# Kernel tuning notes

Hardware: AMD Instinct MI355X
Metric: run time of the kernel (lower is better)

The kernel has to match this reference:

```python
import math
import jax, jax.numpy as jnp
import numpy as np

D = 2048
NH = 16
HD = D // NH
B_IMG = 32
H_ORIG, W_ORIG = 28, 36
POOL = 2
HF, WF = H_ORIG // POOL, W_ORIG // POOL  # 14, 18
T = HF * WF                              # 252 tokens per image
S_TOTAL = B_IMG * T                      # 8064
EPS = 1e-6


def setup_inputs() -> dict:
    key = jax.random.key(0)
    ks = jax.random.split(key, 12)
    w = lambda k, shp: jax.random.normal(k, shp, dtype=jnp.float32) * 0.02
    return {
        'semantic_hidden': jax.random.normal(ks[0], (1, S_TOTAL, D), jnp.float32),
        'vggt_features': jax.random.normal(ks[1], (1, S_TOTAL, D), jnp.float32),
        'grid_thw': jnp.tile(jnp.array([[1, H_ORIG, W_ORIG]], dtype=jnp.int64), (B_IMG, 1)),
        'ln1_w': jnp.ones((D,), jnp.float32), 'ln1_b': jnp.zeros((D,), jnp.float32),
        'ln2_w': jnp.ones((D,), jnp.float32), 'ln2_b': jnp.zeros((D,), jnp.float32),
        'Wq': w(ks[2], (D, D)), 'Wk': w(ks[3], (D, D)),
        'Wv': w(ks[4], (D, D)), 'Wo': w(ks[5], (D, D)),
        'imp_w1': w(ks[6], (D // 4, D)), 'imp_b1': jnp.zeros((D // 4,), jnp.float32),
        'imp_w2': w(ks[7], (1, D // 4)), 'imp_b2': jnp.zeros((1,), jnp.float32),
        'gate_w': w(ks[8], (NH // 2, D)), 'gate_b': jnp.zeros((NH // 2,), jnp.float32),
        'gate': jnp.asarray(0.5, jnp.float32),  # torch init is 0.0 (output would be all-zero); use 0.5 for a meaningful baseline
    }


def _layernorm(x, w, b):
    mu = jnp.mean(x, axis=-1, keepdims=True)
    var = jnp.var(x, axis=-1, keepdims=True)
    return (x - mu) * jax.lax.rsqrt(var + EPS) * w + b


def _spatial_bias(h_feat, w_feat, dtype):
    y = jnp.arange(h_feat, dtype=dtype)
    x = jnp.arange(w_feat, dtype=dtype)
    gy, gx = jnp.meshgrid(y, x, indexing='ij')
    coords = jnp.stack([gy.reshape(-1), gx.reshape(-1)], axis=-1)  # [N, 2]
    diff = coords[:, None, :] - coords[None, :, :]
    dist = jnp.sqrt(jnp.sum(diff * diff, axis=-1))  # [N, N]
    diag_len = math.sqrt(h_feat ** 2 + w_feat ** 2) + 1e-6
    return -dist / diag_len


def reference(semantic_hidden, vggt_features, grid_thw, ln1_w, ln1_b, ln2_w, ln2_b,
              Wq, Wk, Wv, Wo, imp_w1, imp_b1, imp_w2, imp_b2, gate_w, gate_b, gate):
    sem = _layernorm(semantic_hidden, ln1_w, ln1_b)
    vgg = _layernorm(vggt_features, ln2_w, ln2_b)
    B_orig, S_total, Dm = sem.shape

    # grid_thw is a static host constant -> Python ints (shapes must be static)
    h_feat = int(np.asarray(grid_thw)[0, 1]) // POOL
    w_feat = int(np.asarray(grid_thw)[0, 2]) // POOL
    tokens = h_feat * w_feat
    num_images = S_total // tokens

    q_in = sem.reshape(num_images, tokens, Dm)   # [B, S, D]
    kv_in = vgg.reshape(num_images, tokens, Dm)
    B, S = num_images, tokens

    q = (q_in @ Wq.T).reshape(B, S, NH, HD).transpose(0, 2, 1, 3)   # [B, H, S, hd]
    k = (kv_in @ Wk.T).reshape(B, S, NH, HD).transpose(0, 2, 1, 3)
    v = (kv_in @ Wv.T).reshape(B, S, NH, HD).transpose(0, 2, 1, 3)

    attn = jnp.einsum('bhqd,bhkd->bhqk', q, k) / math.sqrt(HD)       # [B, H, S, S]

    # spatial bias on first half of heads, gated per (image, query)
    sp_bias = _spatial_bias(h_feat, w_feat, q.dtype)                 # [S, S]
    gate_score = jax.nn.sigmoid(q_in @ gate_w.T + gate_b)            # [B, S, H/2]
    gate_score = gate_score.transpose(0, 2, 1)[..., None]            # [B, H/2, S, 1]
    split = NH // 2
    attn = attn.at[:, :split].add(sp_bias[None, None] * gate_score)

    # importance gate: log-importance bias over keys, shared across heads
    hidden = jax.nn.relu(q_in @ imp_w1.T + imp_b1)
    importance = jax.nn.sigmoid(hidden @ imp_w2.T + imp_b2)          # [B, S, 1]
    attn = attn + jnp.log(importance + 0.1).reshape(B, 1, 1, S)

    probs = jax.nn.softmax(attn, axis=-1)
    out = jnp.einsum('bhqk,bhkd->bhqd', probs, v)                    # [B, H, S, hd]
    out = out.transpose(0, 2, 1, 3).reshape(B, S, Dm)
    out = out.reshape(B_orig, S_total, Dm) @ Wo.T
    return jnp.tanh(gate) * out
```

## Files before the change

### kernel.cpp

```cpp
#include <hip/hip_runtime.h>
#include <hip/hip_bf16.h>
#include <math.h>

typedef __bf16 bf16_t;
typedef __bf16 bf16x8 __attribute__((ext_vector_type(8)));
typedef float f32x4v __attribute__((ext_vector_type(4)));
typedef unsigned short ushort_t;

#define SL_TOTAL 8064
#define SL_PAD 8192
#define DMODEL 2048
#define NHEAD 16
#define HDIM 128
#define SEQ 252

__device__ __forceinline__ bf16_t f2bf(float f) {
  unsigned u = __builtin_bit_cast(unsigned, f);
  u += 0x7fffu + ((u >> 16) & 1u);
  ushort_t h = (ushort_t)(u >> 16);
  return __builtin_bit_cast(bf16_t, h);
}
__device__ __forceinline__ float bf2f(bf16_t b) {
  unsigned u = ((unsigned)__builtin_bit_cast(ushort_t, b)) << 16;
  return __builtin_bit_cast(float, u);
}

__global__ __launch_bounds__(256) void cvt4_kernel(const float* __restrict__ s0,
                                                   const float* __restrict__ s1,
                                                   const float* __restrict__ s2,
                                                   const float* __restrict__ s3,
                                                   bf16_t* __restrict__ d0,
                                                   bf16_t* __restrict__ d1,
                                                   bf16_t* __restrict__ d2,
                                                   bf16_t* __restrict__ d3) {
  const float* src; bf16_t* dst;
  switch (blockIdx.y) {
    case 0: src = s0; dst = d0; break;
    case 1: src = s1; dst = d1; break;
    case 2: src = s2; dst = d2; break;
    default: src = s3; dst = d3; break;
  }
  int i = (blockIdx.x * 256 + threadIdx.x) * 8;
  float4 a = *(const float4*)(src + i);
  float4 b = *(const float4*)(src + i + 4);
  bf16x8 o;
  o[0] = f2bf(a.x); o[1] = f2bf(a.y); o[2] = f2bf(a.z); o[3] = f2bf(a.w);
  o[4] = f2bf(b.x); o[5] = f2bf(b.y); o[6] = f2bf(b.z); o[7] = f2bf(b.w);
  *(bf16x8*)(dst + i) = o;
}

__global__ __launch_bounds__(256) void cvt_kernel(const float* __restrict__ src,
                                                  bf16_t* __restrict__ dst, int n) {
  int i = (blockIdx.x * 256 + threadIdx.x) * 8;
  if (i >= n) return;
  float4 a = *(const float4*)(src + i);
  float4 b = *(const float4*)(src + i + 4);
  bf16x8 o;
  o[0] = f2bf(a.x); o[1] = f2bf(a.y); o[2] = f2bf(a.z); o[3] = f2bf(a.w);
  o[4] = f2bf(b.x); o[5] = f2bf(b.y); o[6] = f2bf(b.z); o[7] = f2bf(b.w);
  *(bf16x8*)(dst + i) = o;
}

__global__ __launch_bounds__(256) void ln_kernel(
    const float* __restrict__ sem, const float* __restrict__ vgg,
    const float* __restrict__ w1, const float* __restrict__ b1,
    const float* __restrict__ w2, const float* __restrict__ b2,
    bf16_t* __restrict__ o1, bf16_t* __restrict__ o2) {
  const float* x; const float* w; const float* bb; bf16_t* o;
  int row = blockIdx.x;
  if (blockIdx.y == 0) { x = sem; w = w1; bb = b1; o = o1; }
  else                 { x = vgg; w = w2; bb = b2; o = o2; }
  x += (size_t)row * DMODEL; o += (size_t)row * DMODEL;
  int t = threadIdx.x, wid = t >> 6, lane = t & 63;
  float4 va = *(const float4*)(x + t * 8);
  float4 vb = *(const float4*)(x + t * 8 + 4);
  float s  = va.x + va.y + va.z + va.w + vb.x + vb.y + vb.z + vb.w;
  float ss = va.x*va.x + va.y*va.y + va.z*va.z + va.w*va.w
           + vb.x*vb.x + vb.y*vb.y + vb.z*vb.z + vb.w*vb.w;
  #pragma unroll
  for (int m = 1; m < 64; m <<= 1) { s += __shfl_xor(s, m); ss += __shfl_xor(ss, m); }
  __shared__ float rs[4], rss[4];
  if (lane == 0) { rs[wid] = s; rss[wid] = ss; }
  __syncthreads();
  float st = rs[0] + rs[1] + rs[2] + rs[3];
  float sst = rss[0] + rss[1] + rss[2] + rss[3];
  float mu = st * (1.0f / 2048.0f);
  float var = sst * (1.0f / 2048.0f) - mu * mu;
  float rstd = rsqrtf(var + 1e-6f);
  float4 wa = *(const float4*)(w + t * 8);
  float4 wb = *(const float4*)(w + t * 8 + 4);
  float4 ba = *(const float4*)(bb + t * 8);
  float4 bb4 = *(const float4*)(bb + t * 8 + 4);
  bf16x8 ov;
  ov[0] = f2bf((va.x - mu) * rstd * wa.x + ba.x);
  ov[1] = f2bf((va.y - mu) * rstd * wa.y + ba.y);
  ov[2] = f2bf((va.z - mu) * rstd * wa.z + ba.z);
  ov[3] = f2bf((va.w - mu) * rstd * wa.w + ba.w);
  ov[4] = f2bf((vb.x - mu) * rstd * wb.x + bb4.x);
  ov[5] = f2bf((vb.y - mu) * rstd * wb.y + bb4.y);
  ov[6] = f2bf((vb.z - mu) * rstd * wb.z + bb4.z);
  ov[7] = f2bf((vb.w - mu) * rstd * wb.w + bb4.w);
  *(bf16x8*)(o + t * 8) = ov;
}

template <int EPI>
__global__ __launch_bounds__(512, 2) void gemm256(
    const bf16_t* __restrict__ A, const bf16_t* __restrict__ B,
    void* __restrict__ C, void* __restrict__ C2,
    const float* __restrict__ gatep,
    int Mreal, int N, int K, int nnt) {
  __shared__ bf16_t As[2][256 * 64];
  __shared__ bf16_t Bs[2][256 * 64];
  const int nblk = gridDim.x;
  const int orig = blockIdx.x;
  const int qd = nblk >> 3, rr = nblk & 7, xc = orig & 7, lin = orig >> 3;
  const int wg = (xc < rr ? xc * (qd + 1) : rr * (qd + 1) + (xc - rr) * qd) + lin;
  const int mtile = wg / nnt, ntile = wg - mtile * nnt;
  const int m0 = mtile * 256, n0 = ntile * 256;

  const int tid = threadIdx.x;
  const int wid = tid >> 6, lane = tid & 63;
  const int l15 = lane & 15, l4 = lane >> 4;
  const int wr = wid >> 2, wc = wid & 3;
  const int srow = lane >> 3;
  const int scol = 8 * ((lane & 7) ^ srow);

  f32x4v acc[8][4] = {};
  const int NKT = K >> 6;

  auto stage_all = [&](int kt, bf16_t* an, bf16_t* bn) {
    const int k0 = kt << 6;
    #pragma unroll
    for (int it = 0; it < 4; ++it) {
      int chunk = wid + 8 * it;
      int row = chunk * 8 + srow;
      const bf16_t* ga = A + (size_t)(m0 + row) * K + k0 + scol;
      __builtin_amdgcn_global_load_lds((const __attribute__((address_space(1))) unsigned int*)ga,
          (__attribute__((address_space(3))) unsigned int*)(an + chunk * 512), 16, 0, 0);
    }
    #pragma unroll
    for (int it = 0; it < 4; ++it) {
      int chunk = wid + 8 * it;
      int row = chunk * 8 + srow;
      const bf16_t* gb = B + (size_t)(n0 + row) * K + k0 + scol;
      __builtin_amdgcn_global_load_lds((const __attribute__((address_space(1))) unsigned int*)gb,
          (__attribute__((address_space(3))) unsigned int*)(bn + chunk * 512), 16, 0, 0);
    }
  };

  auto ld_a = [&](const bf16_t* as, int ks, int mi) -> bf16x8 {
    int row = wr * 128 + mi * 16 + l15;
    int cb = ks * 64 + l4 * 16;
    return *(const bf16x8*)((const char*)as + row * 128 + (cb ^ ((row & 7) << 4)));
  };
  auto ld_b = [&](const bf16_t* bs, int ks, int ni) -> bf16x8 {
    int row = wc * 64 + ni * 16 + l15;
    int cb = ks * 64 + l4 * 16;
    return *(const bf16x8*)((const char*)bs + row * 128 + (cb ^ ((row & 7) << 4)));
  };

  auto tile_step = [&](int t, const bf16_t* as, const bf16_t* bs,
                       bf16_t* an, bf16_t* bn) {
    bf16x8 af[4], bfv[4];
    #pragma unroll
    for (int mi = 0; mi < 4; ++mi) af[mi] = ld_a(as, 0, mi);
    #pragma unroll
    for (int ni = 0; ni < 4; ++ni) bfv[ni] = ld_b(bs, 0, ni);
    if (t + 1 < NKT) stage_all(t + 1, an, bn);
    __builtin_amdgcn_s_barrier();
    asm volatile("s_waitcnt lgkmcnt(0)" ::: "memory");
    __builtin_amdgcn_sched_barrier(0);
    __builtin_amdgcn_s_setprio(1);
    #pragma unroll
    for (int mi = 0; mi < 4; ++mi)
      #pragma unroll
      for (int ni = 0; ni < 4; ++ni)
        acc[mi][ni] = __builtin_amdgcn_mfma_f32_16x16x32_bf16(af[mi], bfv[ni], acc[mi][ni], 0, 0, 0);
    __builtin_amdgcn_s_setprio(0);
    __builtin_amdgcn_s_barrier();
    __builtin_amdgcn_sched_barrier(0);
    #pragma unroll
    for (int mi = 0; mi < 4; ++mi) af[mi] = ld_a(as, 0, mi + 4);
    __builtin_amdgcn_s_barrier();
    asm volatile("s_waitcnt lgkmcnt(0)" ::: "memory");
    __builtin_amdgcn_sched_barrier(0);
    __builtin_amdgcn_s_setprio(1);
    #pragma unroll
    for (int mi = 0; mi < 4; ++mi)
      #pragma unroll
      for (int ni = 0; ni < 4; ++ni)
        acc[mi + 4][ni] = __builtin_amdgcn_mfma_f32_16x16x32_bf16(af[mi], bfv[ni], acc[mi + 4][ni], 0, 0, 0);
    __builtin_amdgcn_s_setprio(0);
    __builtin_amdgcn_s_barrier();
    __builtin_amdgcn_sched_barrier(0);
    #pragma unroll
    for (int mi = 0; mi < 4; ++mi) af[mi] = ld_a(as, 1, mi);
    #pragma unroll
    for (int ni = 0; ni < 4; ++ni) bfv[ni] = ld_b(bs, 1, ni);
    __builtin_amdgcn_s_barrier();
    asm volatile("s_waitcnt lgkmcnt(0)" ::: "memory");
    __builtin_amdgcn_sched_barrier(0);
    __builtin_amdgcn_s_setprio(1);
    #pragma unroll
    for (int mi = 0; mi < 4; ++mi)
      #pragma unroll
      for (int ni = 0; ni < 4; ++ni)
        acc[mi][ni] = __builtin_amdgcn_mfma_f32_16x16x32_bf16(af[mi], bfv[ni], acc[mi][ni], 0, 0, 0);
    __builtin_amdgcn_s_setprio(0);
    __builtin_amdgcn_s_barrier();
    __builtin_amdgcn_sched_barrier(0);
    #pragma unroll
    for (int mi = 0; mi < 4; ++mi) af[mi] = ld_a(as, 1, mi + 4);
    __builtin_amdgcn_s_barrier();
    asm volatile("s_waitcnt lgkmcnt(0)" ::: "memory");
    __builtin_amdgcn_sched_barrier(0);
    __builtin_amdgcn_s_setprio(1);
    #pragma unroll
    for (int mi = 0; mi < 4; ++mi)
      #pragma unroll
      for (int ni = 0; ni < 4; ++ni)
        acc[mi + 4][ni] = __builtin_amdgcn_mfma_f32_16x16x32_bf16(af[mi], bfv[ni], acc[mi + 4][ni], 0, 0, 0);
    __builtin_amdgcn_s_setprio(0);
    if (t + 1 < NKT) asm volatile("s_waitcnt vmcnt(0)" ::: "memory");
    __builtin_amdgcn_s_barrier();
    __builtin_amdgcn_sched_barrier(0);
  };

  stage_all(0, As[0], Bs[0]);
  asm volatile("s_waitcnt vmcnt(0)" ::: "memory");
  __builtin_amdgcn_s_barrier();
  __builtin_amdgcn_sched_barrier(0);

  for (int t = 0; t < NKT; t += 2) {
    tile_step(t,     As[0], Bs[0], As[1], Bs[1]);
    tile_step(t + 1, As[1], Bs[1], As[0], Bs[0]);
  }

  float scale = 1.0f;
  if (EPI == 2) scale = tanhf(gatep[0]);
  bf16_t* Cb = (bf16_t*)C;
  int colbase = n0;
  int ldc = N;
  if (EPI == 3) {
    ldc = 2048;
    if (n0 >= 2048) { Cb = (bf16_t*)C2; colbase = n0 - 2048; }
  }
  #pragma unroll
  for (int mi = 0; mi < 8; ++mi) {
    #pragma unroll
    for (int ni = 0; ni < 4; ++ni) {
      int c = colbase + wc * 64 + ni * 16 + l15;
      #pragma unroll
      for (int j = 0; j < 4; ++j) {
        int r = m0 + wr * 128 + mi * 16 + 4 * l4 + j;
        if (r >= Mreal) continue;
        float v = acc[mi][ni][j];
        if (EPI == 2) ((float*)C)[(size_t)r * N + c] = v * scale;
        else Cb[(size_t)r * ldc + c] = f2bf(v);
      }
    }
  }
}

template <int EPI>
__global__ __launch_bounds__(256, 2) void gemm_bt(
    const bf16_t* __restrict__ A, const bf16_t* __restrict__ B,
    void* __restrict__ C, void* __restrict__ C2,
    const float* __restrict__ bias, const float* __restrict__ gatep,
    int M, int N, int K, int nnt) {
  __shared__ bf16_t As[2][128 * 64];
  __shared__ bf16_t Bs[2][128 * 64];
  const int nblk = gridDim.x;
  const int orig = blockIdx.x;
  const int qd = nblk >> 3, rr = nblk & 7, xc = orig & 7, lin = orig >> 3;
  const int wg = (xc < rr ? xc * (qd + 1) : rr * (qd + 1) + (xc - rr) * qd) + lin;
  const int mtile = wg / nnt;
  const int ntile = wg - mtile * nnt;
  const int m0 = mtile * 128, n0 = ntile * 128;

  const int tid = threadIdx.x;
  const int wid = tid >> 6, lane = tid & 63;
  const int l15 = lane & 15, l4 = lane >> 4;
  const int wm = (wid >> 1) * 64, wn = (wid & 1) * 64;
  const int srow = lane >> 3;
  const int scol = 8 * ((lane & 7) ^ (lane >> 3));

  f32x4v acc[4][4] = {};
  const int nkt = K >> 6;

  auto stage = [&](int kt, int buf) {
    const int k0 = kt << 6;
    #pragma unroll
    for (int it = 0; it < 4; ++it) {
      int chunk = wid + 4 * it;
      int row = chunk * 8 + srow;
      const bf16_t* ga = A + (size_t)(m0 + row) * K + k0 + scol;
      const bf16_t* gb = B + (size_t)(n0 + row) * K + k0 + scol;
      bf16_t* la = &As[buf][chunk * 512];
      bf16_t* lb = &Bs[buf][chunk * 512];
      __builtin_amdgcn_global_load_lds((const __attribute__((address_space(1))) unsigned int*)ga,
                                       (__attribute__((address_space(3))) unsigned int*)la, 16, 0, 0);
      __builtin_amdgcn_global_load_lds((const __attribute__((address_space(1))) unsigned int*)gb,
                                       (__attribute__((address_space(3))) unsigned int*)lb, 16, 0, 0);
    }
  };

  stage(0, 0);
  for (int kt = 0; kt < nkt; ++kt) {
    int buf = kt & 1;
    __syncthreads();
    if (kt + 1 < nkt) stage(kt + 1, buf ^ 1);
    const char* as = (const char*)As[buf];
    const char* bs = (const char*)Bs[buf];
    #pragma unroll
    for (int ki = 0; ki < 2; ++ki) {
      int cb = ki * 64 + l4 * 16;
      bf16x8 af[4], bfv[4];
      #pragma unroll
      for (int mi = 0; mi < 4; ++mi) {
        int row = wm + mi * 16 + l15;
        af[mi] = *(const bf16x8*)(as + row * 128 + (cb ^ ((row & 7) << 4)));
      }
      #pragma unroll
      for (int ni = 0; ni < 4; ++ni) {
        int row = wn + ni * 16 + l15;
        bfv[ni] = *(const bf16x8*)(bs + row * 128 + (cb ^ ((row & 7) << 4)));
      }
      #pragma unroll
      for (int mi = 0; mi < 4; ++mi)
        #pragma unroll
        for (int ni = 0; ni < 4; ++ni)
          acc[mi][ni] = __builtin_amdgcn_mfma_f32_16x16x32_bf16(af[mi], bfv[ni], acc[mi][ni], 0, 0, 0);
    }
    __syncthreads();
  }

  #pragma unroll
  for (int mi = 0; mi < 4; ++mi) {
    #pragma unroll
    for (int ni = 0; ni < 4; ++ni) {
      int c = n0 + wn + ni * 16 + l15;
      #pragma unroll
      for (int j = 0; j < 4; ++j) {
        int r = m0 + wm + mi * 16 + 4 * l4 + j;
        float v = acc[mi][ni][j];
        if (EPI == 1) { v += bias[c]; v = v > 0.0f ? v : 0.0f; }
        ((bf16_t*)C)[(size_t)r * N + c] = f2bf(v);
      }
    }
  }
}

__global__ __launch_bounds__(256) void gate_kernel(const bf16_t* __restrict__ a,
                                                   const float* __restrict__ gw,
                                                   const float* __restrict__ gb,
                                                   float* __restrict__ gs) {
  int r0 = blockIdx.x * 4;
  int t = threadIdx.x;
  int j = t >> 5, lt = t & 31;
  const float* wr = gw + (size_t)j * DMODEL;
  float sum[4] = {0.0f, 0.0f, 0.0f, 0.0f};
  #pragma unroll
  for (int u = 0; u < 8; ++u) {
    int i = lt * 8 + u * 256;
    float4 w0 = *(const float4*)(wr + i);
    float4 w1 = *(const float4*)(wr + i + 4);
    #pragma unroll
    for (int r = 0; r < 4; ++r) {
      bf16x8 av = *(const bf16x8*)(a + (size_t)(r0 + r) * DMODEL + i);
      sum[r] += bf2f(av[0]) * w0.x + bf2f(av[1]) * w0.y + bf2f(av[2]) * w0.z + bf2f(av[3]) * w0.w
              + bf2f(av[4]) * w1.x + bf2f(av[5]) * w1.y + bf2f(av[6]) * w1.z + bf2f(av[7]) * w1.w;
    }
  }
  #pragma unroll
  for (int m = 1; m < 32; m <<= 1) {
    #pragma unroll
    for (int r = 0; r < 4; ++r) sum[r] += __shfl_xor(sum[r], m);
  }
  if (lt == 0) {
    #pragma unroll
    for (int r = 0; r < 4; ++r)
      gs[(size_t)(r0 + r) * 8 + j] = 1.0f / (1.0f + __expf(-(sum[r] + gb[j])));
  }
}

__global__ __launch_bounds__(256) void imp_kernel(const bf16_t* __restrict__ hid,
                                                  const float* __restrict__ w2,
                                                  const float* __restrict__ b2,
                                                  float* __restrict__ kb) {
  int row = blockIdx.x * 4 + (threadIdx.x >> 6);
  int lane = threadIdx.x & 63;
  const bf16_t* hr = hid + (size_t)row * 512;
  bf16x8 hv = *(const bf16x8*)(hr + lane * 8);
  float sum = 0.0f;
  #pragma unroll
  for (int i = 0; i < 8; ++i) sum += bf2f(hv[i]) * w2[lane * 8 + i];
  #pragma unroll
  for (int m = 1; m < 64; m <<= 1) sum += __shfl_xor(sum, m);
  if (lane == 0) {
    float imp = 1.0f / (1.0f + __expf(-(sum + b2[0])));
    kb[row] = logf(imp + 0.1f);
  }
}

__global__ __launch_bounds__(512, 1) void attn_kernel(
    const bf16_t* __restrict__ Q, const bf16_t* __restrict__ K,
    const bf16_t* __restrict__ V, const float* __restrict__ gs,
    const float* __restrict__ kb, bf16_t* __restrict__ O) {
  __shared__ bf16_t Kt[64 * 128];
  __shared__ bf16_t Vt[128 * 64];
  __shared__ bf16_t Pl[8][32 * 72];
  __shared__ float kyf[256], kxf[256], kbl[256];

  const int bi = blockIdx.x >> 4;
  const int h = blockIdx.x & 15;
  const int tid = threadIdx.x;
  const int wid = tid >> 6;
  const int lane = tid & 63;
  const int l15 = lane & 15, l4 = lane >> 4;
  const bool hs = (h < 8);

  for (int i = tid; i < 256; i += 512) {
    kyf[i] = (float)(i / 18);
    kxf[i] = (float)(i % 18);
    int kk = i < SEQ ? i : SEQ - 1;
    kbl[i] = kb[bi * SEQ + kk];
  }

  const int q0 = wid * 32;
  bf16x8 qf[2][4];
  #pragma unroll
  for (int mi = 0; mi < 2; ++mi) {
    int q = q0 + mi * 16 + l15; if (q >= SEQ) q = SEQ - 1;
    const bf16_t* qp = Q + (size_t)(bi * SEQ + q) * DMODEL + h * HDIM;
    #pragma unroll
    for (int ki = 0; ki < 4; ++ki) qf[mi][ki] = *(const bf16x8*)(qp + ki * 32 + l4 * 8);
  }

  float gsv[2][4], qyv[2][4], qxv[2][4];
  #pragma unroll
  for (int mi = 0; mi < 2; ++mi)
    #pragma unroll
    for (int j = 0; j < 4; ++j) {
      int q = q0 + mi * 16 + 4 * l4 + j;
      int qc = q < SEQ ? q : SEQ - 1;
      gsv[mi][j] = hs ? gs[(size_t)(bi * SEQ + qc) * 8 + h] : 0.0f;
      qyv[mi][j] = (float)(q / 18);
      qxv[mi][j] = (float)(q % 18);
    }

  float mrow[2][4], lrow[2][4];
  #pragma unroll
  for (int mi = 0; mi < 2; ++mi)
    #pragma unroll
    for (int j = 0; j < 4; ++j) { mrow[mi][j] = -3.0e38f; lrow[mi][j] = 0.0f; }

  f32x4v oacc[2][8] = {};
  const float scl = 0.08838834764831845f;
  const float invdiag = 1.0f / (sqrtf(520.0f) + 1e-6f);
  bf16_t* Plw = &Pl[wid][0];

  for (int t = 0; t < 4; ++t) {
    __syncthreads();
    #pragma unroll
    for (int rep = 0; rep < 2; ++rep) {
      int s = tid + rep * 512;
      int row = s >> 4, cb = s & 15;
      int kk = t * 64 + row;
      uint4 val = make_uint4(0, 0, 0, 0);
      if (kk < SEQ) val = *(const uint4*)(K + (size_t)(bi * SEQ + kk) * DMODEL + h * HDIM + cb * 8);
      *(uint4*)((char*)Kt + row * 256 + ((cb * 16) ^ ((row & 7) << 4))) = val;
    }
    {
      int kp = tid >> 4, db = tid & 15;
      int k0i = t * 64 + kp * 2, k1i = k0i + 1;
      uint4 a = make_uint4(0, 0, 0, 0), c4 = make_uint4(0, 0, 0, 0);
      if (k0i < SEQ) a = *(const uint4*)(V + (size_t)(bi * SEQ + k0i) * DMODEL + h * HDIM + db * 8);
      if (k1i < SEQ) c4 = *(const uint4*)(V + (size_t)(bi * SEQ + k1i) * DMODEL + h * HDIM + db * 8);
      const ushort_t* au = (const ushort_t*)&a;
      const ushort_t* cu = (const ushort_t*)&c4;
      #pragma unroll
      for (int i = 0; i < 8; ++i) {
        int d = db * 8 + i;
        unsigned pv = (unsigned)au[i] | ((unsigned)cu[i] << 16);
        *(unsigned*)((char*)Vt + d * 128 + ((kp * 4) ^ ((d & 7) << 4))) = pv;
      }
    }
    __syncthreads();

    f32x4v sc[2][4] = {};
    #pragma unroll
    for (int ki = 0; ki < 4; ++ki) {
      bf16x8 kf[4];
      #pragma unroll
      for (int ni = 0; ni < 4; ++ni) {
        int row = ni * 16 + l15;
        kf[ni] = *(const bf16x8*)((char*)Kt + row * 256 + ((ki * 64 + l4 * 16) ^ ((row & 7) << 4)));
      }
      #pragma unroll
      for (int mi = 0; mi < 2; ++mi)
        #pragma unroll
        for (int ni = 0; ni < 4; ++ni)
          sc[mi][ni] = __builtin_amdgcn_mfma_f32_16x16x32_bf16(qf[mi][ki], kf[ni], sc[mi][ni], 0, 0, 0);
    }

    #pragma unroll
    for (int mi = 0; mi < 2; ++mi) {
      #pragma unroll
      for (int j = 0; j < 4; ++j) {
        float s4[4];
        float rm = -3.0e38f;
        #pragma unroll
        for (int ni = 0; ni < 4; ++ni) {
          int kk = t * 64 + ni * 16 + l15;
          float s = sc[mi][ni][j] * scl + kbl[kk];
          if (hs) {
            float dy = qyv[mi][j] - kyf[kk];
            float dx = qxv[mi][j] - kxf[kk];
            s -= sqrtf(dy * dy + dx * dx) * invdiag * gsv[mi][j];
          }
          if (kk >= SEQ) s = -3.0e38f;
          s4[ni] = s;
          rm = fmaxf(rm, s);
        }
        #pragma unroll
        for (int msk = 1; msk < 16; msk <<= 1) rm = fmaxf(rm, __shfl_xor(rm, msk));
        float mold = mrow[mi][j];
        float mnew = fmaxf(mold, rm);
        float corr = __expf(mold - mnew);
        float rsum = 0.0f;
        #pragma unroll
        for (int ni = 0; ni < 4; ++ni) {
          float p = __expf(s4[ni] - mnew);
          s4[ni] = p;
          rsum += p;
        }
        #pragma unroll
        for (int msk = 1; msk < 16; msk <<= 1) rsum += __shfl_xor(rsum, msk);
        mrow[mi][j] = mnew;
        lrow[mi][j] = lrow[mi][j] * corr + rsum;
        #pragma unroll
        for (int di = 0; di < 8; ++di) oacc[mi][di][j] *= corr;
        int prow = mi * 16 + 4 * l4 + j;
        #pragma unroll
        for (int ni = 0; ni < 4; ++ni)
          Plw[prow * 72 + ni * 16 + l15] = f2bf(s4[ni]);
      }
    }

    #pragma unroll
    for (int ks = 0; ks < 2; ++ks) {
      bf16x8 pf[2];
      #pragma unroll
      for (int mi = 0; mi < 2; ++mi)
        pf[mi] = *(const bf16x8*)(Plw + (mi * 16 + l15) * 72 + ks * 32 + l4 * 8);
      #pragma unroll
      for (int di = 0; di < 8; ++di) {
        int d = di * 16 + l15;
        bf16x8 vf = *(const bf16x8*)((char*)Vt + d * 128 + ((ks * 64 + l4 * 16) ^ ((d & 7) << 4)));
        #pragma unroll
        for (int mi = 0; mi < 2; ++mi)
          oacc[mi][di] = __builtin_amdgcn_mfma_f32_16x16x32_bf16(pf[mi], vf, oacc[mi][di], 0, 0, 0);
      }
    }
  }

  #pragma unroll
  for (int mi = 0; mi < 2; ++mi) {
    #pragma unroll
    for (int j = 0; j < 4; ++j) {
      int q = q0 + mi * 16 + 4 * l4 + j;
      if (q >= SEQ) continue;
      float inv = 1.0f / lrow[mi][j];
      bf16_t* op = O + (size_t)(bi * SEQ + q) * DMODEL + h * HDIM;
      #pragma unroll
      for (int di = 0; di < 8; ++di)
        op[di * 16 + l15] = f2bf(oacc[mi][di][j] * inv);
    }
  }
}

extern "C" void kernel_launch(void* const* d_in, const int* in_sizes, int n_in,
                              void* d_out, int out_size, void* d_ws, size_t ws_size,
                              hipStream_t stream) {
  const float* sem  = (const float*)d_in[0];
  const float* vgg  = (const float*)d_in[1];
  const float* ln1w = (const float*)d_in[3];
  const float* ln1b = (const float*)d_in[4];
  const float* ln2w = (const float*)d_in[5];
  const float* ln2b = (const float*)d_in[6];
  const float* Wq   = (const float*)d_in[7];
  const float* Wk   = (const float*)d_in[8];
  const float* Wv   = (const float*)d_in[9];
  const float* Wo   = (const float*)d_in[10];
  const float* w1   = (const float*)d_in[11];
  const float* b1   = (const float*)d_in[12];
  const float* w2   = (const float*)d_in[13];
  const float* b2   = (const float*)d_in[14];
  const float* gw   = (const float*)d_in[15];
  const float* gb   = (const float*)d_in[16];
  const float* gate = (const float*)d_in[17];

  char* ws = (char*)d_ws;
  const size_t SZ_W    = 8388608;
  const size_t SZ_PAD  = 33554432;
  const size_t SZ_ACT  = 33030144;
  bf16_t* Wqb  = (bf16_t*)(ws + 0);
  bf16_t* Wkb  = (bf16_t*)(ws + SZ_W);
  bf16_t* Wvb  = (bf16_t*)(ws + 2 * SZ_W);
  bf16_t* Wob  = (bf16_t*)(ws + 3 * SZ_W);
  bf16_t* w1b  = (bf16_t*)(ws + 4 * SZ_W);
  bf16_t* semb = (bf16_t*)(ws + 4 * SZ_W + 2097152);
  bf16_t* vggb = (bf16_t*)(ws + 4 * SZ_W + 2097152 + SZ_PAD);
  bf16_t* Vb   = (bf16_t*)(ws + 4 * SZ_W + 2097152 + 2 * SZ_PAD);
  bf16_t* hidb = (bf16_t*)(ws + 4 * SZ_W + 2097152 + 2 * SZ_PAD + SZ_ACT);
  float*  gsb  = (float*)(ws + 4 * SZ_W + 2097152 + 2 * SZ_PAD + SZ_ACT + 8257536);
  float*  kbb  = (float*)(ws + 4 * SZ_W + 2097152 + 2 * SZ_PAD + SZ_ACT + 8257536 + 258048);
  bf16_t* Qb = (bf16_t*)d_out;
  bf16_t* Kb = (bf16_t*)((char*)d_out + SZ_ACT);
  bf16_t* attnb = semb;

  cvt4_kernel<<<dim3(2048, 4), 256, 0, stream>>>(Wq, Wk, Wv, Wo, Wqb, Wkb, Wvb, Wob);
  cvt_kernel<<<512, 256, 0, stream>>>(w1, w1b, 1048576);
  ln_kernel<<<dim3(8064, 2), 256, 0, stream>>>(sem, vgg, ln1w, ln1b, ln2w, ln2b, semb, vggb);

  gemm256<0><<<256, 512, 0, stream>>>(semb, Wqb, Qb, nullptr, nullptr,
                                      8064, 2048, 2048, 8);
  gemm256<3><<<512, 512, 0, stream>>>(vggb, Wkb, Kb, Vb, nullptr,
                                      8064, 4096, 2048, 16);
  gemm_bt<1><<<252, 256, 0, stream>>>(semb, w1b, hidb, nullptr, b1, nullptr,
                                      8064, 512, 2048, 4);

  gate_kernel<<<2016, 256, 0, stream>>>(semb, gw, gb, gsb);
  imp_kernel<<<2016, 256, 0, stream>>>(hidb, w2, b2, kbb);

  attn_kernel<<<512, 512, 0, stream>>>(Qb, Kb, Vb, gsb, kbb, attnb);

  gemm256<2><<<256, 512, 0, stream>>>(attnb, Wob, d_out, nullptr, gate,
                                      8064, 2048, 2048, 8);
}
```

Baseline: 500.3 us.

## Split GEMM tile prefetch into quarter stages interleaved with MFMA phases

Restructures the 256x256 bf16 GEMM main loop so the next k-tile's global-to-LDS loads are issued in four small pieces, two A halves and two B halves, each placed before one MFMA phase. Waits use partial vmcnt counts instead of draining everything at the end of each tile. Each phase loads 8 A fragments and 2 B fragments rather than 4 and 4. The aim is smoother overlap of memory traffic with compute and fewer full pipeline drains. The cost is finer-grained synchronisation that relies on per-wave chunk ownership and vmcnt ordering being correct, which risks reading LDS data before it has landed.

New measurement: 490.3 us. -2.0%, faster.

```diff
diff --git a/kernel.cpp b/kernel.cpp
--- a/kernel.cpp
+++ b/kernel.cpp
@@ -128,26 +128,30 @@
   f32x4v acc[8][4] = {};
   const int NKT = K >> 6;
 
-  auto stage_all = [&](int kt, bf16_t* an, bf16_t* bn) {
+  auto gload = [&](const bf16_t* g, bf16_t* l) {
+    __builtin_amdgcn_global_load_lds((const __attribute__((address_space(1))) unsigned int*)g,
+        (__attribute__((address_space(3))) unsigned int*)l, 16, 0, 0);
+  };
+  auto stageA2 = [&](int kt, int pr) {
+    bf16_t* an = As[kt & 1];
     const int k0 = kt << 6;
     #pragma unroll
-    for (int it = 0; it < 4; ++it) {
-      int chunk = wid + 8 * it;
+    for (int q = 0; q < 2; ++q) {
+      int chunk = wr * 16 + wc * 4 + pr * 2 + q;
       int row = chunk * 8 + srow;
-      const bf16_t* ga = A + (size_t)(m0 + row) * K + k0 + scol;
-      __builtin_amdgcn_global_load_lds((const __attribute__((address_space(1))) unsigned int*)ga,
-          (__attribute__((address_space(3))) unsigned int*)(an + chunk * 512), 16, 0, 0);
-    }
-    #pragma unroll
-    for (int it = 0; it < 4; ++it) {
-      int chunk = wid + 8 * it;
+      gload(A + (size_t)(m0 + row) * K + k0 + scol, an + chunk * 512);
+    }
+  };
+  auto stageB2 = [&](int kt, int nh) {
+    bf16_t* bn = Bs[kt & 1];
+    const int k0 = kt << 6;
+    #pragma unroll
+    for (int q = 0; q < 2; ++q) {
+      int chunk = wc * 8 + nh * 4 + wr * 2 + q;
       int row = chunk * 8 + srow;
-      const bf16_t* gb = B + (size_t)(n0 + row) * K + k0 + scol;
-      __builtin_amdgcn_global_load_lds((const __attribute__((address_space(1))) unsigned int*)gb,
-          (__attribute__((address_space(3))) unsigned int*)(bn + chunk * 512), 16, 0, 0);
+      gload(B + (size_t)(n0 + row) * K + k0 + scol, bn + chunk * 512);
     }
   };
-
   auto ld_a = [&](const bf16_t* as, int ks, int mi) -> bf16x8 {
     int row = wr * 128 + mi * 16 + l15;
     int cb = ks * 64 + l4 * 16;
@@ -159,81 +163,83 @@
     return *(const bf16x8*)((const char*)bs + row * 128 + (cb ^ ((row & 7) << 4)));
   };
 
-  auto tile_step = [&](int t, const bf16_t* as, const bf16_t* bs,
-                       bf16_t* an, bf16_t* bn) {
-    bf16x8 af[4], bfv[4];
-    #pragma unroll
-    for (int mi = 0; mi < 4; ++mi) af[mi] = ld_a(as, 0, mi);
-    #pragma unroll
-    for (int ni = 0; ni < 4; ++ni) bfv[ni] = ld_b(bs, 0, ni);
-    if (t + 1 < NKT) stage_all(t + 1, an, bn);
-    __builtin_amdgcn_s_barrier();
-    asm volatile("s_waitcnt lgkmcnt(0)" ::: "memory");
-    __builtin_amdgcn_sched_barrier(0);
-    __builtin_amdgcn_s_setprio(1);
-    #pragma unroll
-    for (int mi = 0; mi < 4; ++mi)
-      #pragma unroll
-      for (int ni = 0; ni < 4; ++ni)
-        acc[mi][ni] = __builtin_amdgcn_mfma_f32_16x16x32_bf16(af[mi], bfv[ni], acc[mi][ni], 0, 0, 0);
-    __builtin_amdgcn_s_setprio(0);
-    __builtin_amdgcn_s_barrier();
-    __builtin_amdgcn_sched_barrier(0);
-    #pragma unroll
-    for (int mi = 0; mi < 4; ++mi) af[mi] = ld_a(as, 0, mi + 4);
-    __builtin_amdgcn_s_barrier();
-    asm volatile("s_waitcnt lgkmcnt(0)" ::: "memory");
-    __builtin_amdgcn_sched_barrier(0);
-    __builtin_amdgcn_s_setprio(1);
-    #pragma unroll
-    for (int mi = 0; mi < 4; ++mi)
-      #pragma unroll
-      for (int ni = 0; ni < 4; ++ni)
-        acc[mi + 4][ni] = __builtin_amdgcn_mfma_f32_16x16x32_bf16(af[mi], bfv[ni], acc[mi + 4][ni], 0, 0, 0);
-    __builtin_amdgcn_s_setprio(0);
-    __builtin_amdgcn_s_barrier();
-    __builtin_amdgcn_sched_barrier(0);
-    #pragma unroll
-    for (int mi = 0; mi < 4; ++mi) af[mi] = ld_a(as, 1, mi);
-    #pragma unroll
-    for (int ni = 0; ni < 4; ++ni) bfv[ni] = ld_b(bs, 1, ni);
-    __builtin_amdgcn_s_barrier();
-    asm volatile("s_waitcnt lgkmcnt(0)" ::: "memory");
-    __builtin_amdgcn_sched_barrier(0);
-    __builtin_amdgcn_s_setprio(1);
-    #pragma unroll
-    for (int mi = 0; mi < 4; ++mi)
-      #pragma unroll
-      for (int ni = 0; ni < 4; ++ni)
-        acc[mi][ni] = __builtin_amdgcn_mfma_f32_16x16x32_bf16(af[mi], bfv[ni], acc[mi][ni], 0, 0, 0);
-    __builtin_amdgcn_s_setprio(0);
-    __builtin_amdgcn_s_barrier();
-    __builtin_amdgcn_sched_barrier(0);
-    #pragma unroll
-    for (int mi = 0; mi < 4; ++mi) af[mi] = ld_a(as, 1, mi + 4);
-    __builtin_amdgcn_s_barrier();
-    asm volatile("s_waitcnt lgkmcnt(0)" ::: "memory");
-    __builtin_amdgcn_sched_barrier(0);
-    __builtin_amdgcn_s_setprio(1);
-    #pragma unroll
-    for (int mi = 0; mi < 4; ++mi)
-      #pragma unroll
-      for (int ni = 0; ni < 4; ++ni)
-        acc[mi + 4][ni] = __builtin_amdgcn_mfma_f32_16x16x32_bf16(af[mi], bfv[ni], acc[mi + 4][ni], 0, 0, 0);
-    __builtin_amdgcn_s_setprio(0);
-    if (t + 1 < NKT) asm volatile("s_waitcnt vmcnt(0)" ::: "memory");
-    __builtin_amdgcn_s_barrier();
-    __builtin_amdgcn_sched_barrier(0);
-  };
-
-  stage_all(0, As[0], Bs[0]);
-  asm volatile("s_waitcnt vmcnt(0)" ::: "memory");
+  stageA2(0, 0); stageA2(0, 1); stageB2(0, 0); stageB2(0, 1);
+  asm volatile("s_waitcnt vmcnt(2)" ::: "memory");
   __builtin_amdgcn_s_barrier();
   __builtin_amdgcn_sched_barrier(0);
 
-  for (int t = 0; t < NKT; t += 2) {
-    tile_step(t,     As[0], Bs[0], As[1], Bs[1]);
-    tile_step(t + 1, As[1], Bs[1], As[0], Bs[0]);
+  for (int t = 0; t < NKT; ++t) {
+    const bf16_t* as = As[t & 1];
+    const bf16_t* bs = Bs[t & 1];
+    const bool pf = (t + 1 < NKT);
+    bf16x8 afr[8], bfr[2];
+
+    #pragma unroll
+    for (int mi = 0; mi < 8; ++mi) afr[mi] = ld_a(as, 0, mi);
+    bfr[0] = ld_b(bs, 0, 0); bfr[1] = ld_b(bs, 0, 1);
+    if (pf) stageA2(t + 1, 0);
+    __builtin_amdgcn_s_barrier();
+    asm volatile("s_waitcnt lgkmcnt(0)" ::: "memory");
+    __builtin_amdgcn_sched_barrier(0);
+    __builtin_amdgcn_s_setprio(1);
+    #pragma unroll
+    for (int mi = 0; mi < 8; ++mi) {
+      acc[mi][0] = __builtin_amdgcn_mfma_f32_16x16x32_bf16(afr[mi], bfr[0], acc[mi][0], 0, 0, 0);
+      acc[mi][1] = __builtin_amdgcn_mfma_f32_16x16x32_bf16(afr[mi], bfr[1], acc[mi][1], 0, 0, 0);
+    }
+    __builtin_amdgcn_s_setprio(0);
+    if (pf) asm volatile("s_waitcnt vmcnt(2)" ::: "memory");
+    else    asm volatile("s_waitcnt vmcnt(0)" ::: "memory");
+    __builtin_amdgcn_s_barrier();
+    __builtin_amdgcn_sched_barrier(0);
+
+    bfr[0] = ld_b(bs, 0, 2); bfr[1] = ld_b(bs, 0, 3);
+    if (pf) stageA2(t + 1, 1);
+    __builtin_amdgcn_s_barrier();
+    asm volatile("s_waitcnt lgkmcnt(0)" ::: "memory");
+    __builtin_amdgcn_sched_barrier(0);
+    __builtin_amdgcn_s_setprio(1);
+    #pragma unroll
+    for (int mi = 0; mi < 8; ++mi) {
+      acc[mi][2] = __builtin_amdgcn_mfma_f32_16x16x32_bf16(afr[mi], bfr[0], acc[mi][2], 0, 0, 0);
+      acc[mi][3] = __builtin_amdgcn_mfma_f32_16x16x32_bf16(afr[mi], bfr[1], acc[mi][3], 0, 0, 0);
+    }
+    __builtin_amdgcn_s_setprio(0);
+    __builtin_amdgcn_s_barrier();
+    __builtin_amdgcn_sched_barrier(0);
+
+    #pragma unroll
+    for (int mi = 0; mi < 8; ++mi) afr[mi] = ld_a(as, 1, mi);
+    bfr[0] = ld_b(bs, 1, 0); bfr[1] = ld_b(bs, 1, 1);
+    if (pf) stageB2(t + 1, 0);
+    __builtin_amdgcn_s_barrier();
+    asm volatile("s_waitcnt lgkmcnt(0)" ::: "memory");
+    __builtin_amdgcn_sched_barrier(0);
+    __builtin_amdgcn_s_setprio(1);
+    #pragma unroll
+    for (int mi = 0; mi < 8; ++mi) {
+      acc[mi][0] = __builtin_amdgcn_mfma_f32_16x16x32_bf16(afr[mi], bfr[0], acc[mi][0], 0, 0, 0);
+      acc[mi][1] = __builtin_amdgcn_mfma_f32_16x16x32_bf16(afr[mi], bfr[1], acc[mi][1], 0, 0, 0);
+    }
+    __builtin_amdgcn_s_setprio(0);
+    __builtin_amdgcn_s_barrier();
+    __builtin_amdgcn_sched_barrier(0);
+
+    bfr[0] = ld_b(bs, 1, 2); bfr[1] = ld_b(bs, 1, 3);
+    if (pf) stageB2(t + 1, 1);
+    __builtin_amdgcn_s_barrier();
+    asm volatile("s_waitcnt lgkmcnt(0)" ::: "memory");
+    __builtin_amdgcn_sched_barrier(0);
+    __builtin_amdgcn_s_setprio(1);
+    #pragma unroll
+    for (int mi = 0; mi < 8; ++mi) {
+      acc[mi][2] = __builtin_amdgcn_mfma_f32_16x16x32_bf16(afr[mi], bfr[0], acc[mi][2], 0, 0, 0);
+      acc[mi][3] = __builtin_amdgcn_mfma_f32_16x16x32_bf16(afr[mi], bfr[1], acc[mi][3], 0, 0, 0);
+    }
+    __builtin_amdgcn_s_setprio(0);
+    asm volatile("s_waitcnt vmcnt(2)" ::: "memory");
+    __builtin_amdgcn_s_barrier();
+    __builtin_amdgcn_sched_barrier(0);
   }
 
   float scale = 1.0f;
```
